# Kernel tuning notes

Hardware: AMD Instinct MI355X
Metric: run time of the kernel (lower is better)

The kernel has to match this reference:

```python
import jax, jax.numpy as jnp
import numpy as np

B, T, D, E, K = 4, 2048, 2048, 8, 2
H = 4 * D  # expert hidden dim


def setup_inputs() -> dict:
    key = jax.random.key(0)
    ks = jax.random.split(key, 12)
    s = 0.02  # weight init scale
    return {
        "x": jax.random.normal(ks[0], (B, T, D), dtype=jnp.float32),
        "eps": jax.random.normal(ks[1], (B, T, E), dtype=jnp.float32),
        "Wr": jax.random.normal(ks[2], (D, E), dtype=jnp.float32) * s,
        "br": jnp.zeros((E,), dtype=jnp.float32),
        "Wn": jax.random.normal(ks[3], (D, E), dtype=jnp.float32) * s,
        "bn": jnp.zeros((E,), dtype=jnp.float32),
        "W1": jax.random.normal(ks[4], (E, D, H), dtype=jnp.float32) * s,
        "b1": jnp.zeros((E, H), dtype=jnp.float32),
        "W2": jax.random.normal(ks[5], (E, H, D), dtype=jnp.float32) * s,
        "b2": jnp.zeros((E, D), dtype=jnp.float32),
    }


def _moe(x, eps, Wr, br, Wn, bn, W1, b1, W2, b2):
    # --- noisy top-k router ---
    logits = x @ Wr + br                                   # [B,T,E]
    noise_logits = x @ Wn + bn                             # [B,T,E]
    noisy = logits + eps * jax.nn.softplus(noise_logits)   # [B,T,E]
    _, top_idx = jax.lax.top_k(noisy, K)                   # [B,T,K]
    sel = jax.nn.one_hot(top_idx, E, dtype=noisy.dtype).sum(-2)  # [B,T,E] 0/1
    neg_inf = jnp.asarray(-jnp.inf, dtype=noisy.dtype)
    sparse_logits = jnp.where(sel > 0, noisy, neg_inf)
    gates = jax.nn.softmax(sparse_logits, axis=-1)         # zeros off the top-k
    # --- expert MLPs, combined with gates (gate==0 exactly when unrouted,
    #     matching the torch masked gather/scatter; dropout in eval mode) ---
    out = jnp.zeros_like(x)
    for i in range(E):  # fixed small expert count
        h = jax.nn.relu(x @ W1[i] + b1[i])                 # [B,T,H]
        y = h @ W2[i] + b2[i]                              # [B,T,D]
        out = out + y * gates[..., i:i + 1]
    return out


def reference(x, eps, Wr, br, Wn, bn, W1, b1, W2, b2):
    return _moe(x, eps, Wr, br, Wn, bn, W1, b1, W2, b2)
```

## Files before the change

### kernel.cpp

```cpp
#include <hip/hip_runtime.h>

#define BT_TOK 8192
#define DDIM   2048
#define EEXP   8
#define HDIM   8192
#define MAXTILES 72

typedef __bf16 bf16x8 __attribute__((ext_vector_type(8)));
typedef float  f32x4  __attribute__((ext_vector_type(4)));

__device__ inline ushort f2bf(float f) {
  unsigned u = __float_as_uint(f);
  u += 0x7FFFu + ((u >> 16) & 1u);
  return (ushort)(u >> 16);
}

__device__ __forceinline__ void gl16(const ushort* g, ushort* l) {
  __builtin_amdgcn_global_load_lds(
      (const __attribute__((address_space(1))) void*)g,
      (__attribute__((address_space(3))) void*)l, 16, 0, 0);
}

__global__ __launch_bounds__(256) void k_router(
    const float* __restrict__ x, const float* __restrict__ eps,
    const float* __restrict__ Wr, const float* __restrict__ br,
    const float* __restrict__ Wn, const float* __restrict__ bn,
    int* __restrict__ cnt, int* __restrict__ tk_e, int* __restrict__ tk_p,
    float* __restrict__ tk_g)
{
  const int lane = threadIdx.x & 63;
  const int t = blockIdx.x * 4 + (threadIdx.x >> 6);
  const float* xr = x + (size_t)t * DDIM;
  float aL[8] = {0,0,0,0,0,0,0,0};
  float aN[8] = {0,0,0,0,0,0,0,0};
  for (int i = lane; i < DDIM; i += 64) {
    float xv = xr[i];
    const float4* wr4 = (const float4*)(Wr + (size_t)i * EEXP);
    const float4* wn4 = (const float4*)(Wn + (size_t)i * EEXP);
    float4 r0 = wr4[0], r1 = wr4[1];
    float4 n0 = wn4[0], n1 = wn4[1];
    aL[0] += xv * r0.x; aL[1] += xv * r0.y; aL[2] += xv * r0.z; aL[3] += xv * r0.w;
    aL[4] += xv * r1.x; aL[5] += xv * r1.y; aL[6] += xv * r1.z; aL[7] += xv * r1.w;
    aN[0] += xv * n0.x; aN[1] += xv * n0.y; aN[2] += xv * n0.z; aN[3] += xv * n0.w;
    aN[4] += xv * n1.x; aN[5] += xv * n1.y; aN[6] += xv * n1.z; aN[7] += xv * n1.w;
  }
  #pragma unroll
  for (int e = 0; e < 8; ++e) {
    float v = aL[e];
    #pragma unroll
    for (int s = 32; s; s >>= 1) v += __shfl_xor(v, s);
    aL[e] = v;
    float w = aN[e];
    #pragma unroll
    for (int s = 32; s; s >>= 1) w += __shfl_xor(w, s);
    aN[e] = w;
  }
  float nz[8];
  #pragma unroll
  for (int e = 0; e < 8; ++e) {
    float l = aL[e] + br[e];
    float z = aN[e] + bn[e];
    float sp = fmaxf(z, 0.f) + log1pf(expf(-fabsf(z)));
    nz[e] = l + eps[(size_t)t * EEXP + e] * sp;
  }
  int e1 = 0; float v1 = nz[0];
  #pragma unroll
  for (int e = 1; e < 8; ++e) if (nz[e] > v1) { v1 = nz[e]; e1 = e; }
  int e2 = (e1 == 0) ? 1 : 0; float v2 = nz[e2];
  #pragma unroll
  for (int e = 0; e < 8; ++e) if (e != e1 && nz[e] > v2) { v2 = nz[e]; e2 = e; }
  float ex = expf(v2 - v1);
  float g1 = 1.f / (1.f + ex);
  float g2 = ex / (1.f + ex);
  if (lane == 0) {
    int p1 = atomicAdd(&cnt[e1], 1);
    int p2 = atomicAdd(&cnt[e2], 1);
    tk_e[t * 2 + 0] = e1; tk_p[t * 2 + 0] = p1; tk_g[t * 2 + 0] = g1;
    tk_e[t * 2 + 1] = e2; tk_p[t * 2 + 1] = p2; tk_g[t * 2 + 1] = g2;
  }
}

__global__ void k_off(const int* __restrict__ cnt, int* __restrict__ off,
                      int* __restrict__ tileMap, int* __restrict__ nTiles) {
  if (threadIdx.x == 0 && blockIdx.x == 0) {
    int a = 0, nt = 0;
    for (int e = 0; e < EEXP; ++e) {
      off[e] = a;
      int mt = (cnt[e] + 255) >> 8;
      for (int m = 0; m < mt; ++m) tileMap[nt++] = (e << 16) | m;
      a += cnt[e];
    }
    off[EEXP] = a;
    nTiles[0] = nt;
  }
}

__global__ __launch_bounds__(256) void k_gather(
    const float* __restrict__ x, const int* __restrict__ off,
    const int* __restrict__ tk_e, const int* __restrict__ tk_p,
    const float* __restrict__ tk_g,
    int* __restrict__ tok, float* __restrict__ gate, ushort* __restrict__ xg)
{
  const int b = blockIdx.x;
  const int t = b >> 1;
  const int e = tk_e[b];
  const int slot = off[e] + tk_p[b];
  if (threadIdx.x == 0) { tok[slot] = t; gate[slot] = tk_g[b]; }
  const float4* src = (const float4*)(x + (size_t)t * DDIM);
  ushort* dst = xg + (size_t)slot * DDIM;
  const int i = threadIdx.x;
  float4 a = src[i * 2 + 0];
  float4 c = src[i * 2 + 1];
  union { ushort u[8]; uint4 q; } pk;
  pk.u[0] = f2bf(a.x); pk.u[1] = f2bf(a.y); pk.u[2] = f2bf(a.z); pk.u[3] = f2bf(a.w);
  pk.u[4] = f2bf(c.x); pk.u[5] = f2bf(c.y); pk.u[6] = f2bf(c.z); pk.u[7] = f2bf(c.w);
  *(uint4*)(dst + (size_t)i * 8) = pk.q;
}

__global__ __launch_bounds__(256) void k_transpose(
    const float* __restrict__ W, ushort* __restrict__ Wt, int R, int C)
{
  const int e = blockIdx.z;
  const float* We = W + (size_t)e * R * C;
  ushort* Wte = Wt + (size_t)e * R * C;
  const int r0 = blockIdx.y * 64, c0 = blockIdx.x * 64;
  __shared__ float tile[64][65];
  const int tx = threadIdx.x & 15, ty = threadIdx.x >> 4;
  #pragma unroll
  for (int p = 0; p < 4; ++p) {
    float4 v = *(const float4*)(We + (size_t)(r0 + p * 16 + ty) * C + c0 + tx * 4);
    tile[p * 16 + ty][tx * 4 + 0] = v.x;
    tile[p * 16 + ty][tx * 4 + 1] = v.y;
    tile[p * 16 + ty][tx * 4 + 2] = v.z;
    tile[p * 16 + ty][tx * 4 + 3] = v.w;
  }
  __syncthreads();
  const int c = threadIdx.x >> 2, rb = (threadIdx.x & 3) * 16;
  union { ushort u[16]; uint4 q[2]; } pk;
  #pragma unroll
  for (int j = 0; j < 16; ++j) pk.u[j] = f2bf(tile[rb + j][c]);
  uint4* dst = (uint4*)(Wte + (size_t)(c0 + c) * R + r0 + rb);
  dst[0] = pk.q[0];
  dst[1] = pk.q[1];
}


#define MFMA_(a, b, c) __builtin_amdgcn_mfma_f32_16x16x32_bf16(a, b, c, 0, 0, 0)
#define DSR(D, A) asm volatile("ds_read_b128 %0, %1" : "=v"(D) : "v"(A))

#define MQUAD(M, AK0, AK1)                              \
    acc[M][0] = MFMA_(AK0, bv00, acc[M][0]);            \
    acc[M][0] = MFMA_(AK1, bv01, acc[M][0]);            \
    acc[M][1] = MFMA_(AK0, bv10, acc[M][1]);            \
    acc[M][1] = MFMA_(AK1, bv11, acc[M][1]);

#define PHASE(P, ...) do {                                                  \
    bf16x8 av0k0, av0k1, av1k0, av1k1, av2k0, av2k1, av3k0, av3k1;          \
    const int aph = aA + (P) * 8192;                                        \
    DSR(av0k0, aph);        DSR(av0k1, aph ^ 64);                           \
    DSR(av1k0, aph + 2048); DSR(av1k1, (aph + 2048) ^ 64);                  \
    DSR(av2k0, aph + 4096); DSR(av2k1, (aph + 4096) ^ 64);                  \
    DSR(av3k0, aph + 6144); DSR(av3k1, (aph + 6144) ^ 64);                  \
    if ((P) == 0) {                                                         \
      DSR(bv00, bB);        DSR(bv01, bB ^ 64);                             \
      DSR(bv10, bB + 2048); DSR(bv11, (bB + 2048) ^ 64);                    \
    }                                                                       \
    __VA_ARGS__;                                                            \
    __builtin_amdgcn_s_barrier();                                           \
    asm volatile("s_waitcnt lgkmcnt(0)");                                   \
    __builtin_amdgcn_sched_barrier(0);                                      \
    __builtin_amdgcn_s_setprio(1);                                          \
    MQUAD((P)*4 + 0, av0k0, av0k1)                                          \
    MQUAD((P)*4 + 1, av1k0, av1k1)                                          \
    MQUAD((P)*4 + 2, av2k0, av2k1)                                          \
    MQUAD((P)*4 + 3, av3k0, av3k1)                                          \
    __builtin_amdgcn_s_setprio(0);                                          \
  } while (0)

template<int KD, int EPI, int NDIM>
__global__ __launch_bounds__(512, 2) void k_gemm(
    const ushort* __restrict__ A, const ushort* __restrict__ B,
    const float* __restrict__ bias, const int* __restrict__ off,
    const int* __restrict__ tileMap, const int* __restrict__ nTiles,
    const int* __restrict__ tok, const float* __restrict__ gate,
    ushort* __restrict__ Hout, float* __restrict__ Out)
{
  constexpr int NKT = KD / 64;
  __shared__ ushort lds[65536];
  const int bx = blockIdx.x;
  if (bx >= nTiles[0]) return;
  const int em = tileMap[bx];
  const int e = em >> 16, mi = em & 0xffff;
  const int o = off[e], n_e = off[e + 1] - o;
  const int ni = blockIdx.y;
  const int m0 = mi * 256;
  const int tid = threadIdx.x;
  const int lane = tid & 63, wid = tid >> 6;
  const int fr = lane & 15, q = lane >> 4;
  const int wc = wid * 32;

  const ushort* Bex = B + (size_t)e * NDIM * KD;
  const int trow = tid >> 3;
  const int kxor = ((tid & 7) ^ (trow & 7)) * 8;
  const ushort* aS[4]; const ushort* bS[4];
  #pragma unroll
  for (int hj = 0; hj < 4; ++hj) {
    int tr = (hj >> 1) * 128 + (hj & 1) * 64 + trow;
    int ar = m0 + tr; if (ar > n_e - 1) ar = n_e - 1;
    aS[hj] = A + (size_t)(o + ar) * KD + kxor;
    bS[hj] = Bex + (size_t)((size_t)ni * 256 + tr) * KD + kxor;
  }
  const int dstA = tid * 8;
#define STG(SRC, DUS) gl16((SRC), &lds[DUS])

  const unsigned lbase =
      (unsigned)(size_t)(__attribute__((address_space(3))) ushort*)lds;
  const int swzB = (q ^ (fr & 7)) * 16;
  const int aoffB = (int)lbase + fr * 128 + swzB;
  const int boffB = (int)lbase + 32768 + (wc + fr) * 128 + swzB;

  f32x4 acc[16][2];
  #pragma unroll
  for (int m = 0; m < 16; ++m) {
    acc[m][0] = (f32x4){0.f, 0.f, 0.f, 0.f};
    acc[m][1] = (f32x4){0.f, 0.f, 0.f, 0.f};
  }
  bf16x8 bv00, bv01, bv10, bv11;

  STG(bS[0], 16384 + dstA);
  STG(bS[1], 20480 + dstA);
  STG(bS[2], 24576 + dstA);
  STG(bS[3], 28672 + dstA);
  STG(aS[0], 0 + dstA);
  STG(aS[1], 4096 + dstA);
  STG(aS[2], 8192 + dstA);
  STG(aS[3], 12288 + dstA);
  if (NKT > 1) {
    STG(bS[0] + 64, 32768 + 16384 + dstA);
    STG(bS[1] + 64, 32768 + 20480 + dstA);
    STG(bS[2] + 64, 32768 + 24576 + dstA);
    STG(bS[3] + 64, 32768 + 28672 + dstA);
    STG(aS[0] + 64, 32768 + 0 + dstA);
    STG(aS[1] + 64, 32768 + 4096 + dstA);
  }
  if (NKT > 2) asm volatile("s_waitcnt vmcnt(6)");
  else         asm volatile("s_waitcnt vmcnt(0)");
  __builtin_amdgcn_s_barrier();
  __builtin_amdgcn_sched_barrier(0);

  #pragma unroll 1
  for (int t = 0; t < NKT; ++t) {
    const int bbB = (t & 1) << 16;
    const int aA = aoffB + bbB;
    const int bB = boffB + bbB;
    const int cbu = (t & 1) * 32768;
    const int nbu = cbu ^ 32768;

    PHASE(0,
      if (t + 1 < NKT) {
        STG(aS[2] + (size_t)(t + 1) * 64, nbu + 8192 + dstA);
        STG(aS[3] + (size_t)(t + 1) * 64, nbu + 12288 + dstA);
      }
    );
    __builtin_amdgcn_s_barrier();
    PHASE(1,
      if (t + 2 < NKT) {
        STG(bS[0] + (size_t)(t + 2) * 64, cbu + 16384 + dstA);
        STG(bS[1] + (size_t)(t + 2) * 64, cbu + 20480 + dstA);
        STG(bS[2] + (size_t)(t + 2) * 64, cbu + 24576 + dstA);
        STG(bS[3] + (size_t)(t + 2) * 64, cbu + 28672 + dstA);
      }
    );
    __builtin_amdgcn_s_barrier();
    PHASE(2,
      if (t + 2 < NKT) {
        STG(aS[0] + (size_t)(t + 2) * 64, cbu + 0 + dstA);
        STG(aS[1] + (size_t)(t + 2) * 64, cbu + 4096 + dstA);
      }
    );
    __builtin_amdgcn_s_barrier();
    PHASE(3, );
    __builtin_amdgcn_sched_barrier(0);
    if (t >= NKT - 2) asm volatile("s_waitcnt vmcnt(0)");
    else              asm volatile("s_waitcnt vmcnt(6)");
    __builtin_amdgcn_s_barrier();
    __builtin_amdgcn_sched_barrier(0);
  }

  const int colBase = ni * 256 + wc + fr;
  const int rBase = m0 + q * 4;
  const float bb0 = bias[(size_t)e * NDIM + colBase];
  const float bb1 = bias[(size_t)e * NDIM + colBase + 16];

  if constexpr (EPI == 0) {
    #pragma unroll
    for (int m = 0; m < 16; ++m) {
      #pragma unroll
      for (int jj = 0; jj < 4; ++jj) {
        int r = rBase + m * 16 + jj;
        if (r < n_e) {
          ushort* hp = Hout + (size_t)(o + r) * NDIM + colBase;
          hp[0]  = f2bf(fmaxf(acc[m][0][jj] + bb0, 0.f));
          hp[16] = f2bf(fmaxf(acc[m][1][jj] + bb1, 0.f));
        }
      }
    }
  } else {
    #pragma unroll
    for (int m = 0; m < 16; ++m) {
      #pragma unroll
      for (int jj = 0; jj < 4; ++jj) {
        int r = rBase + m * 16 + jj;
        if (r < n_e) {
          int tt = tok[o + r];
          float g = gate[o + r];
          float* op = Out + (size_t)tt * NDIM + colBase;
          atomicAdd(op,      g * (acc[m][0][jj] + bb0));
          atomicAdd(op + 16, g * (acc[m][1][jj] + bb1));
        }
      }
    }
  }
#undef STG
}

extern "C" void kernel_launch(void* const* d_in, const int* in_sizes, int n_in,
                              void* d_out, int out_size, void* d_ws, size_t ws_size,
                              hipStream_t stream) {
  const float* x   = (const float*)d_in[0];
  const float* eps = (const float*)d_in[1];
  const float* Wr  = (const float*)d_in[2];
  const float* br  = (const float*)d_in[3];
  const float* Wn  = (const float*)d_in[4];
  const float* bn  = (const float*)d_in[5];
  const float* W1  = (const float*)d_in[6];
  const float* b1  = (const float*)d_in[7];
  const float* W2  = (const float*)d_in[8];
  const float* b2  = (const float*)d_in[9];
  float* out = (float*)d_out;

  char* p = (char*)d_ws;
  size_t used = 0;
  auto alloc = [&](size_t bytes) -> void* {
    void* r = p + used;
    used += (bytes + 255) & ~(size_t)255;
    return r;
  };
  int*    cnt   = (int*)alloc(EEXP * 4);
  int*    off   = (int*)alloc((EEXP + 1) * 4);
  int*    tmap  = (int*)alloc(MAXTILES * 4);
  int*    ntl   = (int*)alloc(4);
  int*    tk_e  = (int*)alloc(2 * BT_TOK * 4);
  int*    tk_p  = (int*)alloc(2 * BT_TOK * 4);
  float*  tk_g  = (float*)alloc(2 * BT_TOK * 4);
  int*    tok   = (int*)alloc(2 * BT_TOK * 4);
  float*  gate  = (float*)alloc(2 * BT_TOK * 4);
  ushort* xg    = (ushort*)alloc((size_t)2 * BT_TOK * DDIM * 2);
  ushort* Wt1   = (ushort*)alloc((size_t)EEXP * HDIM * DDIM * 2);
  ushort* Wt2   = (ushort*)alloc((size_t)EEXP * HDIM * DDIM * 2);
  ushort* hbuf  = (ushort*)alloc((size_t)2 * BT_TOK * HDIM * 2);
  if (used > ws_size) return;

  hipMemsetAsync(d_out, 0, (size_t)out_size * 4, stream);
  hipMemsetAsync(cnt, 0, EEXP * 4, stream);

  k_router<<<BT_TOK / 4, 256, 0, stream>>>(x, eps, Wr, br, Wn, bn,
                                           cnt, tk_e, tk_p, tk_g);
  k_off<<<1, 64, 0, stream>>>(cnt, off, tmap, ntl);
  k_gather<<<2 * BT_TOK, 256, 0, stream>>>(x, off, tk_e, tk_p, tk_g, tok, gate, xg);

  {
    dim3 g1(HDIM / 64, DDIM / 64, EEXP);
    k_transpose<<<g1, 256, 0, stream>>>(W1, Wt1, DDIM, HDIM);
    dim3 g2(DDIM / 64, HDIM / 64, EEXP);
    k_transpose<<<g2, 256, 0, stream>>>(W2, Wt2, HDIM, DDIM);
  }

  {
    dim3 gg1(MAXTILES, HDIM / 256, 1);
    k_gemm<DDIM, 0, HDIM><<<gg1, 512, 0, stream>>>(xg, Wt1, b1, off, tmap, ntl,
                                                   tok, gate, hbuf, out);
    dim3 gg2(MAXTILES, DDIM / 256, 1);
    k_gemm<HDIM, 1, DDIM><<<gg2, 512, 0, stream>>>(hbuf, Wt2, b2, off, tmap, ntl,
                                                   tok, gate, hbuf, out);
  }
}
```

Measured before the change: 2.002 ms.

## Make grouped GEMM persistent with XCD-aware tile order and 2x4 wave layout

```diff
diff --git a/kernel.cpp b/kernel.cpp
--- a/kernel.cpp
+++ b/kernel.cpp
@@ -148,35 +148,6 @@
 #define MFMA_(a, b, c) __builtin_amdgcn_mfma_f32_16x16x32_bf16(a, b, c, 0, 0, 0)
 #define DSR(D, A) asm volatile("ds_read_b128 %0, %1" : "=v"(D) : "v"(A))
 
-#define MQUAD(M, AK0, AK1)                              \
-    acc[M][0] = MFMA_(AK0, bv00, acc[M][0]);            \
-    acc[M][0] = MFMA_(AK1, bv01, acc[M][0]);            \
-    acc[M][1] = MFMA_(AK0, bv10, acc[M][1]);            \
-    acc[M][1] = MFMA_(AK1, bv11, acc[M][1]);
-
-#define PHASE(P, ...) do {                                                  \
-    bf16x8 av0k0, av0k1, av1k0, av1k1, av2k0, av2k1, av3k0, av3k1;          \
-    const int aph = aA + (P) * 8192;                                        \
-    DSR(av0k0, aph);        DSR(av0k1, aph ^ 64);                           \
-    DSR(av1k0, aph + 2048); DSR(av1k1, (aph + 2048) ^ 64);                  \
-    DSR(av2k0, aph + 4096); DSR(av2k1, (aph + 4096) ^ 64);                  \
-    DSR(av3k0, aph + 6144); DSR(av3k1, (aph + 6144) ^ 64);                  \
-    if ((P) == 0) {                                                         \
-      DSR(bv00, bB);        DSR(bv01, bB ^ 64);                             \
-      DSR(bv10, bB + 2048); DSR(bv11, (bB + 2048) ^ 64);                    \
-    }                                                                       \
-    __VA_ARGS__;                                                            \
-    __builtin_amdgcn_s_barrier();                                           \
-    asm volatile("s_waitcnt lgkmcnt(0)");                                   \
-    __builtin_amdgcn_sched_barrier(0);                                      \
-    __builtin_amdgcn_s_setprio(1);                                          \
-    MQUAD((P)*4 + 0, av0k0, av0k1)                                          \
-    MQUAD((P)*4 + 1, av1k0, av1k1)                                          \
-    MQUAD((P)*4 + 2, av2k0, av2k1)                                          \
-    MQUAD((P)*4 + 3, av3k0, av3k1)                                          \
-    __builtin_amdgcn_s_setprio(0);                                          \
-  } while (0)
-
 template<int KD, int EPI, int NDIM>
 __global__ __launch_bounds__(512, 2) void k_gemm(
     const ushort* __restrict__ A, const ushort* __restrict__ B,
@@ -186,137 +157,203 @@
     ushort* __restrict__ Hout, float* __restrict__ Out)
 {
   constexpr int NKT = KD / 64;
+  constexpr int NTN = NDIM / 256;
   __shared__ ushort lds[65536];
-  const int bx = blockIdx.x;
-  if (bx >= nTiles[0]) return;
-  const int em = tileMap[bx];
-  const int e = em >> 16, mi = em & 0xffff;
-  const int o = off[e], n_e = off[e + 1] - o;
-  const int ni = blockIdx.y;
-  const int m0 = mi * 256;
+  const int TM = nTiles[0];
+  const int T = TM * NTN;
+
+  const int bid = blockIdx.x;
+  const int xcd = bid & 7, slot = bid >> 3;
+  const int qq = T >> 3, rr = T & 7;
+  const int base = xcd * qq + (xcd < rr ? xcd : rr);
+  const int csz = qq + (xcd < rr ? 1 : 0);
+
   const int tid = threadIdx.x;
   const int lane = tid & 63, wid = tid >> 6;
-  const int fr = lane & 15, q = lane >> 4;
-  const int wc = wid * 32;
-
-  const ushort* Bex = B + (size_t)e * NDIM * KD;
-  const int trow = tid >> 3;
-  const int kxor = ((tid & 7) ^ (trow & 7)) * 8;
-  const ushort* aS[4]; const ushort* bS[4];
-  #pragma unroll
-  for (int hj = 0; hj < 4; ++hj) {
-    int tr = (hj >> 1) * 128 + (hj & 1) * 64 + trow;
-    int ar = m0 + tr; if (ar > n_e - 1) ar = n_e - 1;
-    aS[hj] = A + (size_t)(o + ar) * KD + kxor;
-    bS[hj] = Bex + (size_t)((size_t)ni * 256 + tr) * KD + kxor;
-  }
-  const int dstA = tid * 8;
-#define STG(SRC, DUS) gl16((SRC), &lds[DUS])
-
+  const int wm = wid >> 2, wn = wid & 3;
+  const int fr = lane & 15, q2 = lane >> 4;
   const unsigned lbase =
       (unsigned)(size_t)(__attribute__((address_space(3))) ushort*)lds;
-  const int swzB = (q ^ (fr & 7)) * 16;
-  const int aoffB = (int)lbase + fr * 128 + swzB;
-  const int boffB = (int)lbase + 32768 + (wc + fr) * 128 + swzB;
-
-  f32x4 acc[16][2];
-  #pragma unroll
-  for (int m = 0; m < 16; ++m) {
-    acc[m][0] = (f32x4){0.f, 0.f, 0.f, 0.f};
-    acc[m][1] = (f32x4){0.f, 0.f, 0.f, 0.f};
-  }
-  bf16x8 bv00, bv01, bv10, bv11;
-
-  STG(bS[0], 16384 + dstA);
-  STG(bS[1], 20480 + dstA);
-  STG(bS[2], 24576 + dstA);
-  STG(bS[3], 28672 + dstA);
-  STG(aS[0], 0 + dstA);
-  STG(aS[1], 4096 + dstA);
-  STG(aS[2], 8192 + dstA);
-  STG(aS[3], 12288 + dstA);
-  if (NKT > 1) {
-    STG(bS[0] + 64, 32768 + 16384 + dstA);
-    STG(bS[1] + 64, 32768 + 20480 + dstA);
-    STG(bS[2] + 64, 32768 + 24576 + dstA);
-    STG(bS[3] + 64, 32768 + 28672 + dstA);
-    STG(aS[0] + 64, 32768 + 0 + dstA);
-    STG(aS[1] + 64, 32768 + 4096 + dstA);
-  }
-  if (NKT > 2) asm volatile("s_waitcnt vmcnt(6)");
-  else         asm volatile("s_waitcnt vmcnt(0)");
-  __builtin_amdgcn_s_barrier();
-  __builtin_amdgcn_sched_barrier(0);
-
-  #pragma unroll 1
-  for (int t = 0; t < NKT; ++t) {
-    const int bbB = (t & 1) << 16;
-    const int aA = aoffB + bbB;
-    const int bB = boffB + bbB;
-    const int cbu = (t & 1) * 32768;
-    const int nbu = cbu ^ 32768;
-
-    PHASE(0,
-      if (t + 1 < NKT) {
-        STG(aS[2] + (size_t)(t + 1) * 64, nbu + 8192 + dstA);
-        STG(aS[3] + (size_t)(t + 1) * 64, nbu + 12288 + dstA);
-      }
-    );
-    __builtin_amdgcn_s_barrier();
-    PHASE(1,
-      if (t + 2 < NKT) {
-        STG(bS[0] + (size_t)(t + 2) * 64, cbu + 16384 + dstA);
-        STG(bS[1] + (size_t)(t + 2) * 64, cbu + 20480 + dstA);
-        STG(bS[2] + (size_t)(t + 2) * 64, cbu + 24576 + dstA);
-        STG(bS[3] + (size_t)(t + 2) * 64, cbu + 28672 + dstA);
-      }
-    );
-    __builtin_amdgcn_s_barrier();
-    PHASE(2,
-      if (t + 2 < NKT) {
-        STG(aS[0] + (size_t)(t + 2) * 64, cbu + 0 + dstA);
-        STG(aS[1] + (size_t)(t + 2) * 64, cbu + 4096 + dstA);
-      }
-    );
-    __builtin_amdgcn_s_barrier();
-    PHASE(3, );
-    __builtin_amdgcn_sched_barrier(0);
-    if (t >= NKT - 2) asm volatile("s_waitcnt vmcnt(0)");
-    else              asm volatile("s_waitcnt vmcnt(6)");
+  const int swz = (q2 ^ (fr & 7)) * 16;
+  const int aoff0 = (int)lbase + wm * 16384 + fr * 128 + swz;
+  const int boff0 = (int)lbase + 32768 + wn * 8192 + fr * 128 + swz;
+  const int trow = tid >> 3;
+  const int kx = ((tid & 7) ^ (trow & 7)) * 8;
+  const int dstA = tid * 8;
+
+#define STG(SRC, DUS) gl16((SRC), &lds[DUS])
+
+  for (int it = slot; it < csz; it += 32) {
+    const int f = base + it;
+    const int ni = (int)((unsigned)f / (unsigned)TM);
+    const int em = tileMap[f - ni * TM];
+    const int e = em >> 16, mi = em & 0xffff;
+    const int o = off[e], n_e = off[e + 1] - o;
+    const int m0 = mi * 256;
+
+    const ushort* Bex = B + (size_t)e * NDIM * KD + (size_t)ni * 256 * KD;
+    const ushort* aS[4]; const ushort* bS[4];
+    #pragma unroll
+    for (int j = 0; j < 4; ++j) {
+      int ar = m0 + j * 64 + trow;
+      if (ar > n_e - 1) ar = n_e - 1;
+      aS[j] = A + (size_t)(o + ar) * KD + kx;
+      bS[j] = Bex + (size_t)(j * 64 + trow) * KD + kx;
+    }
+
+    f32x4 acc[8][4];
+    #pragma unroll
+    for (int m = 0; m < 8; ++m)
+      #pragma unroll
+      for (int n = 0; n < 4; ++n) acc[m][n] = (f32x4){0.f, 0.f, 0.f, 0.f};
+
+    STG(aS[0], 0 + dstA);        STG(aS[2], 8192 + dstA);
+    STG(aS[1], 4096 + dstA);     STG(aS[3], 12288 + dstA);
+    STG(bS[0], 16384 + dstA);    STG(bS[1], 20480 + dstA);
+    STG(bS[2], 24576 + dstA);    STG(bS[3], 28672 + dstA);
+    if (NKT > 1) {
+      STG(aS[0] + 64, 32768 + 0 + dstA);     STG(aS[2] + 64, 32768 + 8192 + dstA);
+      STG(aS[1] + 64, 32768 + 4096 + dstA);  STG(aS[3] + 64, 32768 + 12288 + dstA);
+      STG(bS[0] + 64, 32768 + 16384 + dstA); STG(bS[1] + 64, 32768 + 20480 + dstA);
+      STG(bS[2] + 64, 32768 + 24576 + dstA); STG(bS[3] + 64, 32768 + 28672 + dstA);
+      asm volatile("s_waitcnt vmcnt(8)");
+    } else {
+      asm volatile("s_waitcnt vmcnt(0)");
+    }
     __builtin_amdgcn_s_barrier();
     __builtin_amdgcn_sched_barrier(0);
-  }
-
-  const int colBase = ni * 256 + wc + fr;
-  const int rBase = m0 + q * 4;
-  const float bb0 = bias[(size_t)e * NDIM + colBase];
-  const float bb1 = bias[(size_t)e * NDIM + colBase + 16];
-
-  if constexpr (EPI == 0) {
+
+    #pragma unroll 1
+    for (int t = 0; t < NKT; ++t) {
+      const int bb = (t & 1) << 16;
+      const int aA = aoff0 + bb;
+      const int bA = boff0 + bb;
+      const int cbu = (t & 1) * 32768;
+      const size_t ko = (size_t)(t + 2) * 64;
+      const bool pf = (t + 2 < NKT);
+
+      bf16x8 avL[8], avH[8], bvL[4], bvH[4];
+
+      #pragma unroll
+      for (int i = 0; i < 4; ++i) {
+        DSR(avL[2 * i],     aA + i * 2048);
+        DSR(avL[2 * i + 1], (aA + i * 2048) ^ 64);
+      }
+      DSR(bvL[0], bA);         DSR(bvL[1], bA ^ 64);
+      DSR(bvL[2], bA + 2048);  DSR(bvL[3], (bA + 2048) ^ 64);
+      __builtin_amdgcn_s_barrier();
+      asm volatile("s_waitcnt lgkmcnt(0)");
+      __builtin_amdgcn_sched_barrier(0);
+      __builtin_amdgcn_s_setprio(1);
+      #pragma unroll
+      for (int i = 0; i < 4; ++i) {
+        acc[i][0] = MFMA_(avL[2 * i], bvL[0], acc[i][0]);
+        acc[i][0] = MFMA_(avL[2 * i + 1], bvL[1], acc[i][0]);
+        acc[i][1] = MFMA_(avL[2 * i], bvL[2], acc[i][1]);
+        acc[i][1] = MFMA_(avL[2 * i + 1], bvL[3], acc[i][1]);
+      }
+      __builtin_amdgcn_s_setprio(0);
+      __builtin_amdgcn_s_barrier();
+
+      #pragma unroll
+      for (int i = 0; i < 4; ++i) {
+        DSR(avH[2 * i],     aA + 8192 + i * 2048);
+        DSR(avH[2 * i + 1], (aA + 8192 + i * 2048) ^ 64);
+      }
+      if (pf) {
+        STG(aS[0] + ko, cbu + 0 + dstA);
+        STG(aS[2] + ko, cbu + 8192 + dstA);
+      }
+      __builtin_amdgcn_s_barrier();
+      asm volatile("s_waitcnt lgkmcnt(0)");
+      __builtin_amdgcn_sched_barrier(0);
+      __builtin_amdgcn_s_setprio(1);
+      #pragma unroll
+      for (int i = 0; i < 4; ++i) {
+        acc[4 + i][0] = MFMA_(avH[2 * i], bvL[0], acc[4 + i][0]);
+        acc[4 + i][0] = MFMA_(avH[2 * i + 1], bvL[1], acc[4 + i][0]);
+        acc[4 + i][1] = MFMA_(avH[2 * i], bvL[2], acc[4 + i][1]);
+        acc[4 + i][1] = MFMA_(avH[2 * i + 1], bvL[3], acc[4 + i][1]);
+      }
+      __builtin_amdgcn_s_setprio(0);
+      __builtin_amdgcn_s_barrier();
+
+      DSR(bvH[0], bA + 4096);  DSR(bvH[1], (bA + 4096) ^ 64);
+      DSR(bvH[2], bA + 6144);  DSR(bvH[3], (bA + 6144) ^ 64);
+      if (pf) {
+        STG(aS[1] + ko, cbu + 4096 + dstA);
+        STG(aS[3] + ko, cbu + 12288 + dstA);
+      }
+      __builtin_amdgcn_s_barrier();
+      asm volatile("s_waitcnt lgkmcnt(0)");
+      __builtin_amdgcn_sched_barrier(0);
+      __builtin_amdgcn_s_setprio(1);
+      #pragma unroll
+      for (int i = 0; i < 4; ++i) {
+        acc[i][2] = MFMA_(avL[2 * i], bvH[0], acc[i][2]);
+        acc[i][2] = MFMA_(avL[2 * i + 1], bvH[1], acc[i][2]);
+        acc[i][3] = MFMA_(avL[2 * i], bvH[2], acc[i][3]);
+        acc[i][3] = MFMA_(avL[2 * i + 1], bvH[3], acc[i][3]);
+      }
+      __builtin_amdgcn_s_setprio(0);
+      __builtin_amdgcn_s_barrier();
+
+      if (pf) {
+        STG(bS[0] + ko, cbu + 16384 + dstA);
+        STG(bS[1] + ko, cbu + 20480 + dstA);
+        STG(bS[2] + ko, cbu + 24576 + dstA);
+        STG(bS[3] + ko, cbu + 28672 + dstA);
+      }
+      __builtin_amdgcn_s_setprio(1);
+      #pragma unroll
+      for (int i = 0; i < 4; ++i) {
+        acc[4 + i][2] = MFMA_(avH[2 * i], bvH[0], acc[4 + i][2]);
+        acc[4 + i][2] = MFMA_(avH[2 * i + 1], bvH[1], acc[4 + i][2]);
+        acc[4 + i][3] = MFMA_(avH[2 * i], bvH[2], acc[4 + i][3]);
+        acc[4 + i][3] = MFMA_(avH[2 * i + 1], bvH[3], acc[4 + i][3]);
+      }
+      __builtin_amdgcn_s_setprio(0);
+      __builtin_amdgcn_sched_barrier(0);
+      if (t < NKT - 2) asm volatile("s_waitcnt vmcnt(8)");
+      else             asm volatile("s_waitcnt vmcnt(0)");
+      __builtin_amdgcn_s_barrier();
+      __builtin_amdgcn_sched_barrier(0);
+    }
+
+    const int colBase = ni * 256 + wn * 64 + fr;
+    const int rBase = m0 + wm * 128 + q2 * 4;
+    float bb4[4];
     #pragma unroll
-    for (int m = 0; m < 16; ++m) {
-      #pragma unroll
-      for (int jj = 0; jj < 4; ++jj) {
-        int r = rBase + m * 16 + jj;
-        if (r < n_e) {
-          ushort* hp = Hout + (size_t)(o + r) * NDIM + colBase;
-          hp[0]  = f2bf(fmaxf(acc[m][0][jj] + bb0, 0.f));
-          hp[16] = f2bf(fmaxf(acc[m][1][jj] + bb1, 0.f));
+    for (int n = 0; n < 4; ++n) bb4[n] = bias[(size_t)e * NDIM + colBase + n * 16];
+
+    if constexpr (EPI == 0) {
+      #pragma unroll
+      for (int m = 0; m < 8; ++m) {
+        #pragma unroll
+        for (int jj = 0; jj < 4; ++jj) {
+          int r = rBase + m * 16 + jj;
+          if (r < n_e) {
+            ushort* hp = Hout + (size_t)(o + r) * NDIM + colBase;
+            #pragma unroll
+            for (int n = 0; n < 4; ++n)
+              hp[n * 16] = f2bf(fmaxf(acc[m][n][jj] + bb4[n], 0.f));
+          }
         }
       }
-    }
-  } else {
-    #pragma unroll
-    for (int m = 0; m < 16; ++m) {
-      #pragma unroll
-      for (int jj = 0; jj < 4; ++jj) {
-        int r = rBase + m * 16 + jj;
-        if (r < n_e) {
-          int tt = tok[o + r];
-          float g = gate[o + r];
-          float* op = Out + (size_t)tt * NDIM + colBase;
-          atomicAdd(op,      g * (acc[m][0][jj] + bb0));
-          atomicAdd(op + 16, g * (acc[m][1][jj] + bb1));
+    } else {
+      #pragma unroll
+      for (int m = 0; m < 8; ++m) {
+        #pragma unroll
+        for (int jj = 0; jj < 4; ++jj) {
+          int r = rBase + m * 16 + jj;
+          if (r < n_e) {
+            int tt = tok[o + r];
+            float g = gate[o + r];
+            float* op = Out + (size_t)tt * NDIM + colBase;
+            #pragma unroll
+            for (int n = 0; n < 4; ++n)
+              atomicAdd(op + n * 16, g * (acc[m][n][jj] + bb4[n]));
+          }
         }
       }
     }
@@ -377,11 +414,9 @@
   }
 
   {
-    dim3 gg1(MAXTILES, HDIM / 256, 1);
-    k_gemm<DDIM, 0, HDIM><<<gg1, 512, 0, stream>>>(xg, Wt1, b1, off, tmap, ntl,
+    k_gemm<DDIM, 0, HDIM><<<256, 512, 0, stream>>>(xg, Wt1, b1, off, tmap, ntl,
                                                    tok, gate, hbuf, out);
-    dim3 gg2(MAXTILES, DDIM / 256, 1);
-    k_gemm<HDIM, 1, DDIM><<<gg2, 512, 0, stream>>>(hbuf, Wt2, b2, off, tmap, ntl,
+    k_gemm<HDIM, 1, DDIM><<<256, 512, 0, stream>>>(hbuf, Wt2, b2, off, tmap, ntl,
                                                    tok, gate, hbuf, out);
   }
 }
```

Measured after the change: 1.918 ms. 4.2% less time.
